# Optimization experiments

Hardware: AMD Instinct MI355X
Metric: run time of the kernel (lower is better)

Reference implementation:

```python
import jax, jax.numpy as jnp
import numpy as np

DIM = 768
HEADS = 12
HEAD_DIM = DIM // HEADS
SCALE = HEAD_DIM ** -0.5
LN_EPS = 1e-5


def setup_inputs() -> dict:
    key = jax.random.key(0)
    ks = jax.random.split(key, 12)
    B, N, C = 8, 1024, DIM
    g = (6.0 / (C + 3 * C)) ** 0.5  # xavier_uniform bound for qkv
    gp = (6.0 / (C + C)) ** 0.5     # xavier_uniform bound for proj
    return {
        "x": jax.random.normal(ks[0], (B, N, C), jnp.float32),
        "w_qkv_id": jax.random.uniform(ks[1], (3 * C, C), jnp.float32, -g, g),
        "w_qkv_cloth": jax.random.uniform(ks[2], (3 * C, C), jnp.float32, -g, g),
        "w_proj_id": jax.random.uniform(ks[3], (C, C), jnp.float32, -gp, gp),
        "b_proj_id": jnp.zeros((C,), jnp.float32),
        "w_proj_cloth": jax.random.uniform(ks[4], (C, C), jnp.float32, -gp, gp),
        "b_proj_cloth": jnp.zeros((C,), jnp.float32),
        "ln_id_w": jnp.ones((C,), jnp.float32),
        "ln_id_b": jnp.zeros((C,), jnp.float32),
        "ln_cloth_w": jnp.ones((C,), jnp.float32),
        "ln_cloth_b": jnp.zeros((C,), jnp.float32),
        "orth_scale": jnp.asarray(0.1, jnp.float32),
    }


def _layernorm(x, w, b):
    mu = jnp.mean(x, axis=-1, keepdims=True)
    var = jnp.var(x, axis=-1, keepdims=True)
    return (x - mu) * jax.lax.rsqrt(var + LN_EPS) * w + b


def _split_heads(qkv, B, N):
    qkv = qkv.reshape(B, N, 3, HEADS, HEAD_DIM).transpose(2, 0, 3, 1, 4)
    return qkv[0], qkv[1], qkv[2]


def _attn(q, k, v):
    s = jnp.einsum("bhnd,bhmd->bhnm", q, k) * SCALE
    s = jnp.clip(s, -20.0, 20.0)
    a = jax.nn.softmax(s, axis=-1)
    a = jnp.where(jnp.isnan(a), jnp.zeros_like(a), a)  # nan guard (dropout = eval/identity)
    return jnp.einsum("bhnm,bhmd->bhnd", a, v)


def reference(x, w_qkv_id, w_qkv_cloth, w_proj_id, b_proj_id, w_proj_cloth,
              b_proj_cloth, ln_id_w, ln_id_b, ln_cloth_w, ln_cloth_b, orth_scale):
    B, N, C = x.shape
    q_id, k_id, v_id = _split_heads(x @ w_qkv_id.T, B, N)
    q_cl, k_cl, v_cl = _split_heads(x @ w_qkv_cloth.T, B, N)

    # Gram-Schmidt orthogonal projection of q_id against q_cloth
    dot = jnp.sum(q_id * q_cl, axis=-1, keepdims=True)          # [B,H,N,1]
    norm_sq = jnp.sum(q_cl * q_cl, axis=-1, keepdims=True) + 1e-5
    coeff = jnp.clip(dot / norm_sq, -1.0, 1.0)
    scale = jnp.clip(orth_scale, 0.0, 1.0)
    q_id_ortho = q_id - scale * (coeff * q_cl)
    saliency = jnp.clip(jnp.mean(jnp.abs(dot) / jnp.sqrt(norm_sq), axis=1), 0.0, 1.0)  # [B,N,1]

    out_id = _attn(q_id_ortho, k_id, v_id).transpose(0, 2, 1, 3).reshape(B, N, C)
    out_cl = _attn(q_cl, k_cl, v_cl).transpose(0, 2, 1, 3).reshape(B, N, C)

    id_feat = _layernorm(out_id @ w_proj_id.T + b_proj_id, ln_id_w, ln_id_b)
    cl_feat = _layernorm(out_cl @ w_proj_cloth.T + b_proj_cloth, ln_cloth_w, ln_cloth_b)
    return id_feat, cl_feat, saliency
```

## Files before the change

### kernel.cpp

```cpp
#include <hip/hip_runtime.h>

typedef unsigned short u16;
typedef short s16x8 __attribute__((ext_vector_type(8)));
typedef float f32x4 __attribute__((ext_vector_type(4)));

#define DEV __device__ __forceinline__

#if __has_builtin(__builtin_amdgcn_exp2f)
#define EXP2F(x) __builtin_amdgcn_exp2f(x)
#else
#define EXP2F(x) exp2f(x)
#endif

DEV u16 f2bf(float f) {
  unsigned int u = __float_as_uint(f);
  u = (u + 0x7fffu + ((u >> 16) & 1u)) >> 16;
  return (u16)u;
}
DEV float bf2f(u16 h) { return __uint_as_float(((unsigned int)h) << 16); }
DEV unsigned int pk_trunc(float lo, float hi) {
  return __builtin_amdgcn_perm(__float_as_uint(hi), __float_as_uint(lo), 0x07060302u);
}

DEV void g2l16(const void* g, void* l) {
  __builtin_amdgcn_global_load_lds(
      (const __attribute__((address_space(1))) unsigned int*)g,
      (__attribute__((address_space(3))) unsigned int*)l, 16, 0, 0);
}

#define SPLANE 6291456

__global__ __launch_bounds__(256) void k_f2bf(const float* __restrict__ in,
                                              u16* __restrict__ out, int n4) {
  int i = blockIdx.x * 256 + threadIdx.x;
  if (i < n4) {
    float4 v = ((const float4*)in)[i];
    ushort4 o;
    o.x = f2bf(v.x); o.y = f2bf(v.y); o.z = f2bf(v.z); o.w = f2bf(v.w);
    ((ushort4*)out)[i] = o;
  }
}

__global__ __launch_bounds__(256) void k_qkv_gemm(const u16* __restrict__ X,
                                                  const u16* __restrict__ Wq,
                                                  u16* __restrict__ QK,
                                                  u16* __restrict__ VT) {
  __shared__ __align__(16) u16 sm[18432];
  u16* lA = sm;
  u16* lB = sm + 4096;
  const int z = blockIdx.z;
  const int n0 = blockIdx.x * 128, m0 = blockIdx.y * 128;
  const u16* W = Wq + (size_t)z * 2304 * 768;
  const int tid = threadIdx.x;
  const int wave = tid >> 6, lane = tid & 63;
  const int wr = (wave >> 1) * 64, wc = (wave & 1) * 64;
  const int fr = lane & 15, fq = lane >> 4;

  f32x4 acc[4][4];
#pragma unroll
  for (int i = 0; i < 4; i++)
#pragma unroll
    for (int j = 0; j < 4; j++) acc[i][j] = (f32x4){0.f, 0.f, 0.f, 0.f};

  for (int k0 = 0; k0 < 768; k0 += 32) {
    __syncthreads();
    {
      int srow = lane >> 2, scol = (lane & 3) * 8;
#pragma unroll
      for (int it = 0; it < 2; ++it) {
        int rb = wave * 32 + it * 16;
        g2l16(X + (size_t)(m0 + rb + srow) * 768 + k0 + scol, &lA[rb * 32]);
        g2l16(W + (size_t)(n0 + rb + srow) * 768 + k0 + scol, &lB[rb * 32]);
      }
    }
    __syncthreads();
    s16x8 af[4], bfr[4];
#pragma unroll
    for (int i = 0; i < 4; i++) af[i] = *(const s16x8*)&lB[(wc + i * 16 + fr) * 32 + fq * 8];
#pragma unroll
    for (int j = 0; j < 4; j++) bfr[j] = *(const s16x8*)&lA[(wr + j * 16 + fr) * 32 + fq * 8];
#pragma unroll
    for (int i = 0; i < 4; i++)
#pragma unroll
      for (int j = 0; j < 4; j++)
        acc[i][j] = __builtin_amdgcn_mfma_f32_16x16x32_bf16(af[i], bfr[j], acc[i][j], 0, 0, 0);
  }

  __syncthreads();
  u16* ep = sm + wave * 4608;
#pragma unroll
  for (int i = 0; i < 4; i++)
#pragma unroll
    for (int j = 0; j < 4; j++) {
      unsigned int lo = (unsigned int)f2bf(acc[i][j][0]) | ((unsigned int)f2bf(acc[i][j][1]) << 16);
      unsigned int hi = (unsigned int)f2bf(acc[i][j][2]) | ((unsigned int)f2bf(acc[i][j][3]) << 16);
      uint2 pk; pk.x = lo; pk.y = hi;
      *(uint2*)&ep[(j * 16 + fr) * 72 + i * 16 + fq * 4] = pk;
    }
  __builtin_amdgcn_s_waitcnt(0);

  const int c0 = n0 + wc;
  const int t0 = m0 + wr;
  const int b = t0 >> 10, tt0 = t0 & 1023;
  if (c0 < 1536) {
    const int three = (c0 >= 768) ? 1 : 0;
    const int h = (c0 - three * 768) >> 6;
    u16* dst = QK + ((size_t)z * 2 + three) * SPLANE +
               ((size_t)(b * 12 + h) * 1024 + tt0) * 64;
#pragma unroll
    for (int pass = 0; pass < 8; ++pass) {
      int row = pass * 8 + (lane >> 3);
      int dch = (lane & 7) * 8;
      *(uint4*)&dst[(size_t)row * 64 + dch] = *(const uint4*)&ep[row * 72 + dch];
    }
  } else {
    const int h = (c0 - 1536) >> 6;
    u16* dst = VT + (size_t)z * SPLANE + ((size_t)(b * 12 + h) * 64) * 1024 + tt0;
#pragma unroll
    for (int pass = 0; pass < 8; ++pass) {
      int d = pass * 8 + (lane >> 3);
      int tch = (lane & 7) * 8;
      unsigned int w0[4];
#pragma unroll
      for (int k2 = 0; k2 < 4; k2++) {
        unsigned int lo = ep[(tch + k2 * 2) * 72 + d];
        unsigned int hi = ep[(tch + k2 * 2 + 1) * 72 + d];
        w0[k2] = lo | (hi << 16);
      }
      uint4 val;
      val.x = w0[0]; val.y = w0[1]; val.z = w0[2]; val.w = w0[3];
      *(uint4*)&dst[(size_t)d * 1024 + tch] = val;
    }
  }
}

__global__ __launch_bounds__(256) void k_ortho(u16* __restrict__ QK,
                                               const float* __restrict__ orth_scale,
                                               float* __restrict__ sal) {
  const int wave = threadIdx.x >> 6, lane = threadIdx.x & 63;
  const int row = blockIdx.x * 4 + wave;
  const int b = row >> 10, n = row & 1023;
  const float scale = fminf(fmaxf(orth_scale[0], 0.f), 1.f);
  u16* qid = QK;
  u16* qcl = QK + (size_t)2 * SPLANE;
  float sacc = 0.f;
  for (int h = 0; h < 12; ++h) {
    size_t off = (((size_t)(b * 12 + h)) * 1024 + n) * 64 + lane;
    float qi = bf2f(qid[off]);
    float qc = bf2f(qcl[off]);
    float d = qi * qc, nq = qc * qc;
#pragma unroll
    for (int s = 1; s < 64; s <<= 1) { d += __shfl_xor(d, s); nq += __shfl_xor(nq, s); }
    nq += 1e-5f;
    float coeff = fminf(fmaxf(d / nq, -1.f), 1.f);
    qid[off] = f2bf(qi - scale * coeff * qc);
    sacc += fabsf(d) / sqrtf(nq);
  }
  if (lane == 0) sal[row] = fminf(fmaxf(sacc * (1.f / 12.f), 0.f), 1.f);
}

#define AST 72
#define PST 40
__global__ __launch_bounds__(256, 3) void k_attn(const u16* __restrict__ QK,
                                                 const u16* __restrict__ VT,
                                                 u16* __restrict__ aout) {
  __shared__ __align__(16) u16 sm[19456];
  u16* lK = sm;
  u16* lVT = sm + 4608;
  const int z = blockIdx.z, bh = blockIdx.y;
  const int q0 = blockIdx.x * 256;
  const int b = bh / 12, hd = bh - b * 12;
  const size_t plane = (size_t)bh * 65536;
  const u16* Q  = QK + (size_t)z * 2 * SPLANE + plane;
  const u16* K  = QK + ((size_t)z * 2 + 1) * SPLANE + plane;
  const u16* Vt = VT + (size_t)z * SPLANE + plane;

  const int tid = threadIdx.x, wave = tid >> 6, lane = tid & 63;
  const int fr = lane & 15, fq = lane >> 4;
  u16* lP = sm + 9216 + wave * 2560;

  s16x8 qf[4][2];
#pragma unroll
  for (int s = 0; s < 4; s++) {
    const u16* qrow = Q + (size_t)(q0 + wave * 64 + s * 16 + fr) * 64;
    qf[s][0] = *(const s16x8*)&qrow[fq * 8];
    qf[s][1] = *(const s16x8*)&qrow[32 + fq * 8];
  }

  f32x4 oacc[4][4];
  float lsum[4];
#pragma unroll
  for (int s = 0; s < 4; s++) {
    lsum[s] = 0.f;
#pragma unroll
    for (int j = 0; j < 4; j++) oacc[s][j] = (f32x4){0.f, 0.f, 0.f, 0.f};
  }

  const int srow = tid >> 3, sc8 = (tid & 7) * 8;

  for (int kv0 = 0; kv0 < 1024; kv0 += 64) {
    __syncthreads();
    {
      const u16* kb = K + (size_t)kv0 * 64;
      *(uint4*)&lK[srow * AST + sc8]        = *(const uint4*)&kb[(size_t)srow * 64 + sc8];
      *(uint4*)&lK[(srow + 32) * AST + sc8] = *(const uint4*)&kb[(size_t)(srow + 32) * 64 + sc8];
      const u16* vb = Vt + kv0;
      *(uint4*)&lVT[srow * AST + sc8]        = *(const uint4*)&vb[(size_t)srow * 1024 + sc8];
      *(uint4*)&lVT[(srow + 32) * AST + sc8] = *(const uint4*)&vb[(size_t)(srow + 32) * 1024 + sc8];
    }
    __syncthreads();

#pragma unroll
    for (int ph = 0; ph < 2; ++ph) {
#pragma unroll
      for (int jh = 0; jh < 2; ++jh) {
        const int jt = ph * 2 + jh;
        s16x8 kf0 = *(const s16x8*)&lK[(jt * 16 + fr) * AST + fq * 8];
        s16x8 kf1 = *(const s16x8*)&lK[(jt * 16 + fr) * AST + 32 + fq * 8];
#pragma unroll
        for (int s = 0; s < 4; s++) {
          f32x4 t = (f32x4){0.f, 0.f, 0.f, 0.f};
          t = __builtin_amdgcn_mfma_f32_16x16x32_bf16(kf0, qf[s][0], t, 0, 0, 0);
          t = __builtin_amdgcn_mfma_f32_16x16x32_bf16(kf1, qf[s][1], t, 0, 0, 0);
          float p0 = EXP2F(fmaf(t[0], 0.18033688f, -28.8539008f));
          float p1 = EXP2F(fmaf(t[1], 0.18033688f, -28.8539008f));
          float p2 = EXP2F(fmaf(t[2], 0.18033688f, -28.8539008f));
          float p3 = EXP2F(fmaf(t[3], 0.18033688f, -28.8539008f));
          lsum[s] += (p0 + p1) + (p2 + p3);
          uint2 pk; pk.x = pk_trunc(p0, p1); pk.y = pk_trunc(p2, p3);
          *(uint2*)&lP[(s * 16 + fr) * PST + jh * 16 + fq * 4] = pk;
        }
      }
      __builtin_amdgcn_s_waitcnt(0);
      s16x8 pa[4];
#pragma unroll
      for (int s = 0; s < 4; s++) pa[s] = *(const s16x8*)&lP[(s * 16 + fr) * PST + fq * 8];
#pragma unroll
      for (int jt = 0; jt < 4; jt++) {
        s16x8 vb = *(const s16x8*)&lVT[(jt * 16 + fr) * AST + ph * 32 + fq * 8];
#pragma unroll
        for (int s = 0; s < 4; s++)
          oacc[s][jt] = __builtin_amdgcn_mfma_f32_16x16x32_bf16(pa[s], vb, oacc[s][jt], 0, 0, 0);
      }
    }
  }

#pragma unroll
  for (int s = 0; s < 4; s++) {
    float v = lsum[s];
    v += __shfl_xor(v, 16);
    v += __shfl_xor(v, 32);
    lsum[s] = v;
  }
#pragma unroll
  for (int s = 0; s < 4; s++) {
#pragma unroll
    for (int r = 0; r < 4; r++) {
      float inv = 1.f / __shfl(lsum[s], fq * 4 + r);
      int t = q0 + wave * 64 + s * 16 + fq * 4 + r;
      size_t base = ((size_t)z * 8192 + b * 1024 + t) * 768 + hd * 64 + fr;
#pragma unroll
      for (int jt = 0; jt < 4; jt++)
        aout[base + jt * 16] = f2bf(oacc[s][jt][r] * inv);
    }
  }
}

__global__ __launch_bounds__(256) void k_proj_gemm(const u16* __restrict__ A,
                                                   const u16* __restrict__ Wp,
                                                   const float* __restrict__ bias_id,
                                                   const float* __restrict__ bias_cl,
                                                   u16* __restrict__ out) {
  __shared__ __align__(16) u16 sm[18432];
  u16* lA = sm;
  u16* lB = sm + 4096;
  const int z = blockIdx.z;
  const int n0 = blockIdx.x * 128, m0 = blockIdx.y * 128;
  const u16* Az = A + (size_t)z * 8192 * 768;
  const u16* Wz = Wp + (size_t)z * 768 * 768;
  const float* bias = z ? bias_cl : bias_id;
  u16* oz = out + (size_t)z * 8192 * 768;
  const int tid = threadIdx.x;
  const int wave = tid >> 6, lane = tid & 63;
  const int wr = (wave >> 1) * 64, wc = (wave & 1) * 64;
  const int fr = lane & 15, fq = lane >> 4;

  float bv[4][4];
#pragma unroll
  for (int i = 0; i < 4; i++)
#pragma unroll
    for (int r = 0; r < 4; r++) bv[i][r] = bias[n0 + wc + i * 16 + fq * 4 + r];

  f32x4 acc[4][4];
#pragma unroll
  for (int i = 0; i < 4; i++)
#pragma unroll
    for (int j = 0; j < 4; j++) acc[i][j] = (f32x4){0.f, 0.f, 0.f, 0.f};

  for (int k0 = 0; k0 < 768; k0 += 32) {
    __syncthreads();
    {
      int srow = lane >> 2, scol = (lane & 3) * 8;
#pragma unroll
      for (int it = 0; it < 2; ++it) {
        int rb = wave * 32 + it * 16;
        g2l16(Az + (size_t)(m0 + rb + srow) * 768 + k0 + scol, &lA[rb * 32]);
        g2l16(Wz + (size_t)(n0 + rb + srow) * 768 + k0 + scol, &lB[rb * 32]);
      }
    }
    __syncthreads();
    s16x8 af[4], bfr[4];
#pragma unroll
    for (int i = 0; i < 4; i++) af[i] = *(const s16x8*)&lB[(wc + i * 16 + fr) * 32 + fq * 8];
#pragma unroll
    for (int j = 0; j < 4; j++) bfr[j] = *(const s16x8*)&lA[(wr + j * 16 + fr) * 32 + fq * 8];
#pragma unroll
    for (int i = 0; i < 4; i++)
#pragma unroll
      for (int j = 0; j < 4; j++)
        acc[i][j] = __builtin_amdgcn_mfma_f32_16x16x32_bf16(af[i], bfr[j], acc[i][j], 0, 0, 0);
  }

  __syncthreads();
  u16* ep = sm + wave * 4608;
#pragma unroll
  for (int i = 0; i < 4; i++)
#pragma unroll
    for (int j = 0; j < 4; j++) {
      unsigned int lo = (unsigned int)f2bf(acc[i][j][0] + bv[i][0]) |
                        ((unsigned int)f2bf(acc[i][j][1] + bv[i][1]) << 16);
      unsigned int hi = (unsigned int)f2bf(acc[i][j][2] + bv[i][2]) |
                        ((unsigned int)f2bf(acc[i][j][3] + bv[i][3]) << 16);
      uint2 pk; pk.x = lo; pk.y = hi;
      *(uint2*)&ep[(j * 16 + fr) * 72 + i * 16 + fq * 4] = pk;
    }
  __builtin_amdgcn_s_waitcnt(0);

  const int c0 = n0 + wc;
#pragma unroll
  for (int pass = 0; pass < 8; ++pass) {
    int row = pass * 8 + (lane >> 3);
    int dch = (lane & 7) * 8;
    u16* dst = oz + (size_t)(m0 + wr + row) * 768 + c0;
    *(uint4*)&dst[dch] = *(const uint4*)&ep[row * 72 + dch];
  }
}

__global__ __launch_bounds__(256) void k_ln(const u16* __restrict__ pin,
                                            const float* __restrict__ w_id,
                                            const float* __restrict__ b_id,
                                            const float* __restrict__ w_cl,
                                            const float* __restrict__ b_cl,
                                            float* __restrict__ out) {
  __shared__ float red[2][8];
  const int row = blockIdx.x;
  const int z = row >> 13;
  const float* w = z ? w_cl : w_id;
  const float* bb = z ? b_cl : b_id;
  const u16* x = pin + (size_t)row * 768;
  float v[3];
  float s = 0.f, s2 = 0.f;
#pragma unroll
  for (int i = 0; i < 3; i++) {
    v[i] = bf2f(x[threadIdx.x + i * 256]);
    s += v[i];
    s2 += v[i] * v[i];
  }
#pragma unroll
  for (int sh = 1; sh < 64; sh <<= 1) { s += __shfl_xor(s, sh); s2 += __shfl_xor(s2, sh); }
  const int wave = threadIdx.x >> 6, lane = threadIdx.x & 63;
  if (lane == 0) { red[0][wave] = s; red[1][wave] = s2; }
  __syncthreads();
  s = red[0][0] + red[0][1] + red[0][2] + red[0][3];
  s2 = red[1][0] + red[1][1] + red[1][2] + red[1][3];
  float mu = s * (1.f / 768.f);
  float var = s2 * (1.f / 768.f) - mu * mu;
  float rstd = rsqrtf(fmaxf(var, 0.f) + 1e-5f);
  float* o = out + (size_t)row * 768;
#pragma unroll
  for (int i = 0; i < 3; i++) {
    int c = threadIdx.x + i * 256;
    o[c] = (v[i] - mu) * rstd * w[c] + bb[c];
  }
}

extern "C" void kernel_launch(void* const* d_in, const int* in_sizes, int n_in,
                              void* d_out, int out_size, void* d_ws, size_t ws_size,
                              hipStream_t stream) {
  const float* x        = (const float*)d_in[0];
  const float* w_qkv_id = (const float*)d_in[1];
  const float* w_qkv_cl = (const float*)d_in[2];
  const float* w_proj_id= (const float*)d_in[3];
  const float* b_proj_id= (const float*)d_in[4];
  const float* w_proj_cl= (const float*)d_in[5];
  const float* b_proj_cl= (const float*)d_in[6];
  const float* ln_id_w  = (const float*)d_in[7];
  const float* ln_id_b  = (const float*)d_in[8];
  const float* ln_cl_w  = (const float*)d_in[9];
  const float* ln_cl_b  = (const float*)d_in[10];
  const float* orth     = (const float*)d_in[11];
  float* out = (float*)d_out;

  u16* xb    = (u16*)d_ws;
  u16* wqkv  = xb + 6291456;
  u16* wproj = wqkv + 3538944;
  u16* qk    = wproj + 1179648;
  u16* vt    = qk + 25165824;
  u16* aout  = vt + 12582912;
  u16* pout  = qk;

  k_f2bf<<<6144, 256, 0, stream>>>(x, xb, 1572864);
  k_f2bf<<<1728, 256, 0, stream>>>(w_qkv_id, wqkv, 442368);
  k_f2bf<<<1728, 256, 0, stream>>>(w_qkv_cl, wqkv + 1769472, 442368);
  k_f2bf<<<576, 256, 0, stream>>>(w_proj_id, wproj, 147456);
  k_f2bf<<<576, 256, 0, stream>>>(w_proj_cl, wproj + 589824, 147456);

  k_qkv_gemm<<<dim3(18, 64, 2), 256, 0, stream>>>(xb, wqkv, qk, vt);
  k_ortho<<<2048, 256, 0, stream>>>(qk, orth, out + 12582912);
  k_attn<<<dim3(4, 96, 2), 256, 0, stream>>>(qk, vt, aout);
  k_proj_gemm<<<dim3(6, 64, 2), 256, 0, stream>>>(aout, wproj, b_proj_id, b_proj_cl, pout);
  k_ln<<<16384, 256, 0, stream>>>(pout, ln_id_w, ln_id_b, ln_cl_w, ln_cl_b, out);
}
```

Measured before the change: 335.1 us.

## Merge fp32-to-bf16 conversions, widen GEMM K-tile with XOR swizzle, prefetch attention KV

The five conversion launches become one kernel that picks its source buffer from the global thread index. Both GEMMs now stage a 64-wide K tile with an XOR-swizzled LDS layout, which halves the barrier count and avoids bank conflicts on fragment reads. The attention kernel loads the next K/V tile into registers while the current tile is being computed, hiding global latency at the cost of extra registers. The prefetch wraps around and re-reads the first tile on the last iteration, which is a redundant load.

```diff
diff --git a/kernel.cpp b/kernel.cpp
--- a/kernel.cpp
+++ b/kernel.cpp
@@ -30,15 +30,26 @@
 
 #define SPLANE 6291456
 
-__global__ __launch_bounds__(256) void k_f2bf(const float* __restrict__ in,
-                                              u16* __restrict__ out, int n4) {
+__global__ __launch_bounds__(256) void k_cvt(const float* __restrict__ x,
+                                             const float* __restrict__ wqi,
+                                             const float* __restrict__ wqc,
+                                             const float* __restrict__ wpi,
+                                             const float* __restrict__ wpc,
+                                             u16* __restrict__ xb,
+                                             u16* __restrict__ wqkv,
+                                             u16* __restrict__ wproj) {
   int i = blockIdx.x * 256 + threadIdx.x;
-  if (i < n4) {
-    float4 v = ((const float4*)in)[i];
-    ushort4 o;
-    o.x = f2bf(v.x); o.y = f2bf(v.y); o.z = f2bf(v.z); o.w = f2bf(v.w);
-    ((ushort4*)out)[i] = o;
-  }
+  const float* src; u16* dst; int off;
+  if (i < 1572864)      { src = x;   dst = xb;             off = 0; }
+  else if (i < 2015232) { src = wqi; dst = wqkv;           off = 1572864; }
+  else if (i < 2457600) { src = wqc; dst = wqkv + 1769472; off = 2015232; }
+  else if (i < 2605056) { src = wpi; dst = wproj;          off = 2457600; }
+  else                  { src = wpc; dst = wproj + 589824; off = 2605056; }
+  int j = i - off;
+  float4 v = ((const float4*)src)[j];
+  ushort4 o;
+  o.x = f2bf(v.x); o.y = f2bf(v.y); o.z = f2bf(v.z); o.w = f2bf(v.w);
+  ((ushort4*)dst)[j] = o;
 }
 
 __global__ __launch_bounds__(256) void k_qkv_gemm(const u16* __restrict__ X,
@@ -47,7 +58,7 @@
                                                   u16* __restrict__ VT) {
   __shared__ __align__(16) u16 sm[18432];
   u16* lA = sm;
-  u16* lB = sm + 4096;
+  u16* lB = sm + 8192;
   const int z = blockIdx.z;
   const int n0 = blockIdx.x * 128, m0 = blockIdx.y * 128;
   const u16* W = Wq + (size_t)z * 2304 * 768;
@@ -62,28 +73,37 @@
 #pragma unroll
     for (int j = 0; j < 4; j++) acc[i][j] = (f32x4){0.f, 0.f, 0.f, 0.f};
 
-  for (int k0 = 0; k0 < 768; k0 += 32) {
-    __syncthreads();
-    {
-      int srow = lane >> 2, scol = (lane & 3) * 8;
-#pragma unroll
-      for (int it = 0; it < 2; ++it) {
-        int rb = wave * 32 + it * 16;
-        g2l16(X + (size_t)(m0 + rb + srow) * 768 + k0 + scol, &lA[rb * 32]);
-        g2l16(W + (size_t)(n0 + rb + srow) * 768 + k0 + scol, &lB[rb * 32]);
-      }
-    }
-    __syncthreads();
-    s16x8 af[4], bfr[4];
-#pragma unroll
-    for (int i = 0; i < 4; i++) af[i] = *(const s16x8*)&lB[(wc + i * 16 + fr) * 32 + fq * 8];
-#pragma unroll
-    for (int j = 0; j < 4; j++) bfr[j] = *(const s16x8*)&lA[(wr + j * 16 + fr) * 32 + fq * 8];
-#pragma unroll
-    for (int i = 0; i < 4; i++)
-#pragma unroll
-      for (int j = 0; j < 4; j++)
-        acc[i][j] = __builtin_amdgcn_mfma_f32_16x16x32_bf16(af[i], bfr[j], acc[i][j], 0, 0, 0);
+  const int srow = lane >> 3;
+  const int scol = ((lane & 7) ^ srow) * 8;
+
+  for (int k0 = 0; k0 < 768; k0 += 64) {
+    __syncthreads();
+#pragma unroll
+    for (int it = 0; it < 4; ++it) {
+      int rb = wave * 32 + it * 8;
+      g2l16(X + (size_t)(m0 + rb + srow) * 768 + k0 + scol, &lA[rb * 64]);
+      g2l16(W + (size_t)(n0 + rb + srow) * 768 + k0 + scol, &lB[rb * 64]);
+    }
+    __syncthreads();
+#pragma unroll
+    for (int ks = 0; ks < 2; ++ks) {
+      s16x8 af[4], bfr[4];
+#pragma unroll
+      for (int i = 0; i < 4; i++) {
+        int row = wc + i * 16 + fr;
+        af[i] = *(const s16x8*)&lB[row * 64 + (((ks * 4 + fq) ^ (row & 7)) * 8)];
+      }
+#pragma unroll
+      for (int j = 0; j < 4; j++) {
+        int row = wr + j * 16 + fr;
+        bfr[j] = *(const s16x8*)&lA[row * 64 + (((ks * 4 + fq) ^ (row & 7)) * 8)];
+      }
+#pragma unroll
+      for (int i = 0; i < 4; i++)
+#pragma unroll
+        for (int j = 0; j < 4; j++)
+          acc[i][j] = __builtin_amdgcn_mfma_f32_16x16x32_bf16(af[i], bfr[j], acc[i][j], 0, 0, 0);
+    }
   }
 
   __syncthreads();
@@ -198,17 +218,28 @@
 
   const int srow = tid >> 3, sc8 = (tid & 7) * 8;
 
+  uint4 rk0 = *(const uint4*)&K[(size_t)srow * 64 + sc8];
+  uint4 rk1 = *(const uint4*)&K[(size_t)(srow + 32) * 64 + sc8];
+  uint4 rv0 = *(const uint4*)&Vt[(size_t)srow * 1024 + sc8];
+  uint4 rv1 = *(const uint4*)&Vt[(size_t)(srow + 32) * 1024 + sc8];
+
   for (int kv0 = 0; kv0 < 1024; kv0 += 64) {
     __syncthreads();
+    *(uint4*)&lK[srow * AST + sc8]         = rk0;
+    *(uint4*)&lK[(srow + 32) * AST + sc8]  = rk1;
+    *(uint4*)&lVT[srow * AST + sc8]        = rv0;
+    *(uint4*)&lVT[(srow + 32) * AST + sc8] = rv1;
+    __syncthreads();
+
     {
-      const u16* kb = K + (size_t)kv0 * 64;
-      *(uint4*)&lK[srow * AST + sc8]        = *(const uint4*)&kb[(size_t)srow * 64 + sc8];
-      *(uint4*)&lK[(srow + 32) * AST + sc8] = *(const uint4*)&kb[(size_t)(srow + 32) * 64 + sc8];
-      const u16* vb = Vt + kv0;
-      *(uint4*)&lVT[srow * AST + sc8]        = *(const uint4*)&vb[(size_t)srow * 1024 + sc8];
-      *(uint4*)&lVT[(srow + 32) * AST + sc8] = *(const uint4*)&vb[(size_t)(srow + 32) * 1024 + sc8];
-    }
-    __syncthreads();
+      int nxt = (kv0 + 64) & 1023;
+      const u16* kb = K + (size_t)nxt * 64;
+      rk0 = *(const uint4*)&kb[(size_t)srow * 64 + sc8];
+      rk1 = *(const uint4*)&kb[(size_t)(srow + 32) * 64 + sc8];
+      const u16* vb = Vt + nxt;
+      rv0 = *(const uint4*)&vb[(size_t)srow * 1024 + sc8];
+      rv1 = *(const uint4*)&vb[(size_t)(srow + 32) * 1024 + sc8];
+    }
 
 #pragma unroll
     for (int ph = 0; ph < 2; ++ph) {
@@ -273,7 +304,7 @@
                                                    u16* __restrict__ out) {
   __shared__ __align__(16) u16 sm[18432];
   u16* lA = sm;
-  u16* lB = sm + 4096;
+  u16* lB = sm + 8192;
   const int z = blockIdx.z;
   const int n0 = blockIdx.x * 128, m0 = blockIdx.y * 128;
   const u16* Az = A + (size_t)z * 8192 * 768;
@@ -297,28 +328,37 @@
 #pragma unroll
     for (int j = 0; j < 4; j++) acc[i][j] = (f32x4){0.f, 0.f, 0.f, 0.f};
 
-  for (int k0 = 0; k0 < 768; k0 += 32) {
-    __syncthreads();
-    {
-      int srow = lane >> 2, scol = (lane & 3) * 8;
-#pragma unroll
-      for (int it = 0; it < 2; ++it) {
-        int rb = wave * 32 + it * 16;
-        g2l16(Az + (size_t)(m0 + rb + srow) * 768 + k0 + scol, &lA[rb * 32]);
-        g2l16(Wz + (size_t)(n0 + rb + srow) * 768 + k0 + scol, &lB[rb * 32]);
-      }
-    }
-    __syncthreads();
-    s16x8 af[4], bfr[4];
-#pragma unroll
-    for (int i = 0; i < 4; i++) af[i] = *(const s16x8*)&lB[(wc + i * 16 + fr) * 32 + fq * 8];
-#pragma unroll
-    for (int j = 0; j < 4; j++) bfr[j] = *(const s16x8*)&lA[(wr + j * 16 + fr) * 32 + fq * 8];
-#pragma unroll
-    for (int i = 0; i < 4; i++)
-#pragma unroll
-      for (int j = 0; j < 4; j++)
-        acc[i][j] = __builtin_amdgcn_mfma_f32_16x16x32_bf16(af[i], bfr[j], acc[i][j], 0, 0, 0);
+  const int srow = lane >> 3;
+  const int scol = ((lane & 7) ^ srow) * 8;
+
+  for (int k0 = 0; k0 < 768; k0 += 64) {
+    __syncthreads();
+#pragma unroll
+    for (int it = 0; it < 4; ++it) {
+      int rb = wave * 32 + it * 8;
+      g2l16(Az + (size_t)(m0 + rb + srow) * 768 + k0 + scol, &lA[rb * 64]);
+      g2l16(Wz + (size_t)(n0 + rb + srow) * 768 + k0 + scol, &lB[rb * 64]);
+    }
+    __syncthreads();
+#pragma unroll
+    for (int ks = 0; ks < 2; ++ks) {
+      s16x8 af[4], bfr[4];
+#pragma unroll
+      for (int i = 0; i < 4; i++) {
+        int row = wc + i * 16 + fr;
+        af[i] = *(const s16x8*)&lB[row * 64 + (((ks * 4 + fq) ^ (row & 7)) * 8)];
+      }
+#pragma unroll
+      for (int j = 0; j < 4; j++) {
+        int row = wr + j * 16 + fr;
+        bfr[j] = *(const s16x8*)&lA[row * 64 + (((ks * 4 + fq) ^ (row & 7)) * 8)];
+      }
+#pragma unroll
+      for (int i = 0; i < 4; i++)
+#pragma unroll
+        for (int j = 0; j < 4; j++)
+          acc[i][j] = __builtin_amdgcn_mfma_f32_16x16x32_bf16(af[i], bfr[j], acc[i][j], 0, 0, 0);
+    }
   }
 
   __syncthreads();
@@ -409,12 +449,8 @@
   u16* aout  = vt + 12582912;
   u16* pout  = qk;
 
-  k_f2bf<<<6144, 256, 0, stream>>>(x, xb, 1572864);
-  k_f2bf<<<1728, 256, 0, stream>>>(w_qkv_id, wqkv, 442368);
-  k_f2bf<<<1728, 256, 0, stream>>>(w_qkv_cl, wqkv + 1769472, 442368);
-  k_f2bf<<<576, 256, 0, stream>>>(w_proj_id, wproj, 147456);
-  k_f2bf<<<576, 256, 0, stream>>>(w_proj_cl, wproj + 589824, 147456);
-
+  k_cvt<<<10752, 256, 0, stream>>>(x, w_qkv_id, w_qkv_cl, w_proj_id, w_proj_cl,
+                                   xb, wqkv, wproj);
   k_qkv_gemm<<<dim3(18, 64, 2), 256, 0, stream>>>(xb, wqkv, qk, vt);
   k_ortho<<<2048, 256, 0, stream>>>(qk, orth, out + 12582912);
   k_attn<<<dim3(4, 96, 2), 256, 0, stream>>>(qk, vt, aout);
```

Result: no change. 331.3 us (-1.2%).
